# Kernel tuning notes

Measured on AMD Instinct MI355X. Metric: run time of the kernel, lower is better.

## Reference

```python
import jax, jax.numpy as jnp
import numpy as np

VOCAB = 50257
CH = 1024          # c_hidden_size = hidden_size(1020) + class_num(4)
LAT = 128
T = 1024
EOS = 1


def setup_inputs() -> dict:
    key = jax.random.key(0)
    ks = jax.random.split(key, 12)
    s = 0.02
    # tokens in [2, VOCAB) so EOS only appears at the final position
    toks = jax.random.randint(ks[0], (T,), 2, VOCAB, dtype=jnp.int32)
    input_tensor = toks.at[-1].set(EOS)
    inp = {
        "input_tensor": input_tensor,
        "h0": jnp.zeros((1, 1, CH), jnp.float32),
        "c0": jnp.zeros((1, 1, CH), jnp.float32),
        "eps": jax.random.normal(ks[1], (1, 1, LAT), jnp.float32),
        "emb": jax.random.normal(ks[2], (VOCAB, CH), jnp.float32) * s,
        "W_ih": jax.random.normal(ks[3], (4 * CH, CH), jnp.float32) * s,
        "W_hh": jax.random.normal(ks[4], (4 * CH, CH), jnp.float32) * s,
        "b_ih": jax.random.normal(ks[5], (4 * CH,), jnp.float32) * s,
        "b_hh": jax.random.normal(ks[6], (4 * CH,), jnp.float32) * s,
        "W_mean": jax.random.normal(ks[7], (LAT, 2 * CH), jnp.float32) * s,
        "b_mean": jnp.zeros((LAT,), jnp.float32),
        "W_logv": jax.random.normal(ks[8], (LAT, 2 * CH), jnp.float32) * s,
        "b_logv": jnp.zeros((LAT,), jnp.float32),
    }
    return inp


def reference(input_tensor, h0, c0, eps, emb, W_ih, W_hh, b_ih, b_hh,
              W_mean, b_mean, W_logv, b_logv):
    Tlen = input_tensor.shape[0]
    eos_idx = jnp.argmax(input_tensor == EOS)           # first EOS position
    active = jnp.arange(Tlen) < eos_idx                 # steps taken before break
    x_all = emb[input_tensor]                            # [T, CH]

    def step(carry, inp):
        h, c = carry
        x, a = inp
        gates = x @ W_ih.T + b_ih + h @ W_hh.T + b_hh    # [4*CH]
        i, f, g, o = jnp.split(gates, 4)                 # PyTorch LSTM gate order
        c_new = jax.nn.sigmoid(f) * c + jax.nn.sigmoid(i) * jnp.tanh(g)
        h_new = jax.nn.sigmoid(o) * jnp.tanh(c_new)
        h = jnp.where(a, h_new, h)
        c = jnp.where(a, c_new, c)
        return (h, c), None

    (h, c), _ = jax.lax.scan(step, (h0.reshape(-1), c0.reshape(-1)), (x_all, active))
    hc = jnp.concatenate([h, c])                         # cat((h, c), dim=2) flattened
    mean = hc @ W_mean.T + b_mean
    logv = hc @ W_logv.T + b_logv
    z = eps.reshape(-1) * jnp.exp(0.5 * logv) + mean     # reparameterize
    shp = (1, 1, LAT)
    return z.reshape(shp), mean.reshape(shp), logv.reshape(shp)
```

## Files before the change

### kernel.cpp

```cpp
#include <hip/hip_runtime.h>
#include <cstdint>
#include <cstddef>

#define T_LEN 1024
#define CH    1024
#define NGATE 4096
#define LAT   128
#define NBLK  128

#define WS_XG    0
#define WS_HBUF  (16777216)
#define WS_HFIN  (16777216 + 16384)
#define WS_CFIN  (16777216 + 24576)
#define WS_CTRL  (16777216 + 32768)

__device__ __forceinline__ float sigmf(float x) { return 1.0f / (1.0f + expf(-x)); }

__global__ __launch_bounds__(1024) void setup_k(const int* __restrict__ tok,
                                                int* __restrict__ ctrl) {
  __shared__ int red[1024];
  int tid = threadIdx.x;
  red[tid] = (tok[tid] == 1) ? tid : 0x7fffffff;
  __syncthreads();
  for (int s = 512; s > 0; s >>= 1) {
    if (tid < s) red[tid] = min(red[tid], red[tid + s]);
    __syncthreads();
  }
  if (tid == 0) {
    int e = red[0];
    ctrl[0] = (e == 0x7fffffff) ? 0 : e;
  }
}

__global__ __launch_bounds__(512) void xgemm_k(const int* __restrict__ tok,
                                               const float* __restrict__ emb,
                                               const float* __restrict__ Wih,
                                               const float* __restrict__ bih,
                                               const float* __restrict__ bhh,
                                               float* __restrict__ xg) {
  __shared__ float As[16 * 132];
  __shared__ float Bs[16 * 132];
  const int tid = threadIdx.x;
  const int r0 = blockIdx.x * 128;
  const int t0 = blockIdx.y * 128;
  const int tx = tid & 15, ty = tid >> 4;
  const int m0 = ty * 4, n0 = tx * 8;
  const int lrow = tid >> 2;
  const int kq   = (tid & 3) * 4;

  float acc[4][8];
#pragma unroll
  for (int i = 0; i < 4; i++)
#pragma unroll
    for (int j = 0; j < 8; j++) acc[i][j] = 0.0f;

  const int tokv = tok[t0 + lrow];
  const float* arow = emb + (size_t)tokv * CH;
  const float* brow = Wih + (size_t)(r0 + lrow) * CH;

  for (int k0 = 0; k0 < CH; k0 += 16) {
    float4 a4 = *(const float4*)(arow + k0 + kq);
    float4 b4 = *(const float4*)(brow + k0 + kq);
    __syncthreads();
    As[(kq + 0) * 132 + lrow] = a4.x;
    As[(kq + 1) * 132 + lrow] = a4.y;
    As[(kq + 2) * 132 + lrow] = a4.z;
    As[(kq + 3) * 132 + lrow] = a4.w;
    Bs[(kq + 0) * 132 + lrow] = b4.x;
    Bs[(kq + 1) * 132 + lrow] = b4.y;
    Bs[(kq + 2) * 132 + lrow] = b4.z;
    Bs[(kq + 3) * 132 + lrow] = b4.w;
    __syncthreads();
#pragma unroll
    for (int kk = 0; kk < 16; kk++) {
      float4 av = *(const float4*)&As[kk * 132 + m0];
      float4 b0 = *(const float4*)&Bs[kk * 132 + n0];
      float4 b1 = *(const float4*)&Bs[kk * 132 + n0 + 4];
      float aa[4] = {av.x, av.y, av.z, av.w};
      float bb[8] = {b0.x, b0.y, b0.z, b0.w, b1.x, b1.y, b1.z, b1.w};
#pragma unroll
      for (int i = 0; i < 4; i++)
#pragma unroll
        for (int j = 0; j < 8; j++) acc[i][j] += aa[i] * bb[j];
    }
  }

  float4 bi0 = *(const float4*)(bih + r0 + n0);
  float4 bi1 = *(const float4*)(bih + r0 + n0 + 4);
  float4 bh0 = *(const float4*)(bhh + r0 + n0);
  float4 bh1 = *(const float4*)(bhh + r0 + n0 + 4);
  float badd[8] = {bi0.x + bh0.x, bi0.y + bh0.y, bi0.z + bh0.z, bi0.w + bh0.w,
                   bi1.x + bh1.x, bi1.y + bh1.y, bi1.z + bh1.z, bi1.w + bh1.w};
#pragma unroll
  for (int i = 0; i < 4; i++) {
    float4 o0 = {acc[i][0] + badd[0], acc[i][1] + badd[1],
                 acc[i][2] + badd[2], acc[i][3] + badd[3]};
    float4 o1 = {acc[i][4] + badd[4], acc[i][5] + badd[5],
                 acc[i][6] + badd[6], acc[i][7] + badd[7]};
    float* dst = xg + (size_t)(t0 + m0 + i) * NGATE + r0 + n0;
    *(float4*)(dst) = o0;
    *(float4*)(dst + 4) = o1;
  }
}

__global__ __launch_bounds__(1024) void lstm_k(const float* __restrict__ h0,
                                               const float* __restrict__ c0,
                                               const float* __restrict__ eps,
                                               const float* __restrict__ Whh,
                                               const float* __restrict__ Wm,
                                               const float* __restrict__ bm,
                                               const float* __restrict__ Wl,
                                               const float* __restrict__ bl,
                                               const float* __restrict__ xg,
                                               unsigned long long* __restrict__ hbuf64,
                                               unsigned long long* __restrict__ hfin64,
                                               unsigned long long* __restrict__ cfin64,
                                               const int* __restrict__ ctrl,
                                               float* __restrict__ out) {
  __shared__ float hs[1024];
  __shared__ float hcs[2048];
  __shared__ float gv[32];
  __shared__ float rs[32];

  const int tid = threadIdx.x;
  const int b = blockIdx.x;
  const int g = tid >> 5, s = tid & 31;
  const int q = g >> 3, jj = g & 7;
  const int r = q * 1024 + b * 8 + jj;

  const float* wrow = Whh + (size_t)r * CH;
  float w[32];
#pragma unroll
  for (int i = 0; i < 32; i++) w[i] = wrow[s + 32 * i];

  const int eos = ctrl[0];

  float hreg = 0.0f, creg = 0.0f;
  if (tid < 8) { hreg = h0[b * 8 + tid]; creg = c0[b * 8 + tid]; }

  for (int t = 0; t < eos; t++) {
    float xv = 0.0f;
    if (s == 0) xv = xg[(size_t)t * NGATE + r];

    if (t == 0) {
      hs[tid] = h0[tid];
    } else {
      const unsigned want = (unsigned)t;
      const unsigned long long* src = hbuf64 + (size_t)(t & 1) * 1024 + tid;
      unsigned long long v;
      do {
        v = __hip_atomic_load(src, __ATOMIC_RELAXED, __HIP_MEMORY_SCOPE_AGENT);
      } while ((unsigned)(v >> 32) != want);
      hs[tid] = __uint_as_float((unsigned)(v & 0xffffffffu));
    }
    __syncthreads();

    float a0 = 0.0f, a1 = 0.0f;
#pragma unroll
    for (int i = 0; i < 32; i += 2) {
      a0 += w[i]     * hs[s + 32 * i];
      a1 += w[i + 1] * hs[s + 32 * (i + 1)];
    }
    float acc = a0 + a1;
    acc += __shfl_xor(acc, 16);
    acc += __shfl_xor(acc, 8);
    acc += __shfl_xor(acc, 4);
    acc += __shfl_xor(acc, 2);
    acc += __shfl_xor(acc, 1);
    if (s == 0) gv[g] = acc + xv;
    __syncthreads();

    if (tid < 8) {
      float iv = gv[tid], fv = gv[8 + tid], gg = gv[16 + tid], ov = gv[24 + tid];
      float cn = sigmf(fv) * creg + sigmf(iv) * tanhf(gg);
      float hn = sigmf(ov) * tanhf(cn);
      creg = cn; hreg = hn;
      unsigned long long pv = ((unsigned long long)(unsigned)(t + 1) << 32) |
                              (unsigned long long)__float_as_uint(hn);
      __hip_atomic_store(&hbuf64[(size_t)((t + 1) & 1) * 1024 + b * 8 + tid], pv,
                         __ATOMIC_RELAXED, __HIP_MEMORY_SCOPE_AGENT);
    }
  }

  if (tid < 8) {
    unsigned long long ph = (1ull << 32) | (unsigned long long)__float_as_uint(hreg);
    unsigned long long pc = (1ull << 32) | (unsigned long long)__float_as_uint(creg);
    __hip_atomic_store(&hfin64[b * 8 + tid], ph, __ATOMIC_RELAXED, __HIP_MEMORY_SCOPE_AGENT);
    __hip_atomic_store(&cfin64[b * 8 + tid], pc, __ATOMIC_RELAXED, __HIP_MEMORY_SCOPE_AGENT);
  }

  {
    unsigned long long vh, vc;
    do {
      vh = __hip_atomic_load(&hfin64[tid], __ATOMIC_RELAXED, __HIP_MEMORY_SCOPE_AGENT);
    } while ((unsigned)(vh >> 32) != 1u);
    do {
      vc = __hip_atomic_load(&cfin64[tid], __ATOMIC_RELAXED, __HIP_MEMORY_SCOPE_AGENT);
    } while ((unsigned)(vc >> 32) != 1u);
    hcs[tid] = __uint_as_float((unsigned)(vh & 0xffffffffu));
    hcs[1024 + tid] = __uint_as_float((unsigned)(vc & 0xffffffffu));
  }
  __syncthreads();

  float hc1 = hcs[tid];
  float hc2 = hcs[1024 + tid];
  float pm = Wm[(size_t)b * 2048 + tid] * hc1 + Wm[(size_t)b * 2048 + 1024 + tid] * hc2;
  float pl = Wl[(size_t)b * 2048 + tid] * hc1 + Wl[(size_t)b * 2048 + 1024 + tid] * hc2;
#pragma unroll
  for (int o = 32; o > 0; o >>= 1) {
    pm += __shfl_down(pm, o);
    pl += __shfl_down(pl, o);
  }
  const int wv = tid >> 6, ln = tid & 63;
  if (ln == 0) { rs[wv] = pm; rs[16 + wv] = pl; }
  __syncthreads();
  if (tid == 0) {
    float m = 0.0f, l = 0.0f;
    for (int i = 0; i < 16; i++) { m += rs[i]; l += rs[16 + i]; }
    m += bm[b];
    l += bl[b];
    float z = eps[b] * expf(0.5f * l) + m;
    out[b] = z;
    out[LAT + b] = m;
    out[2 * LAT + b] = l;
  }
}

extern "C" void kernel_launch(void* const* d_in, const int* in_sizes, int n_in,
                              void* d_out, int out_size, void* d_ws, size_t ws_size,
                              hipStream_t stream) {
  const int*   tok = (const int*)d_in[0];
  const float* h0  = (const float*)d_in[1];
  const float* c0  = (const float*)d_in[2];
  const float* eps = (const float*)d_in[3];
  const float* emb = (const float*)d_in[4];
  const float* Wih = (const float*)d_in[5];
  const float* Whh = (const float*)d_in[6];
  const float* bih = (const float*)d_in[7];
  const float* bhh = (const float*)d_in[8];
  const float* Wm  = (const float*)d_in[9];
  const float* bm  = (const float*)d_in[10];
  const float* Wl  = (const float*)d_in[11];
  const float* bl  = (const float*)d_in[12];
  float* out = (float*)d_out;

  char* ws = (char*)d_ws;
  float* xg = (float*)(ws + WS_XG);
  unsigned long long* hbuf64 = (unsigned long long*)(ws + WS_HBUF);
  unsigned long long* hfin64 = (unsigned long long*)(ws + WS_HFIN);
  unsigned long long* cfin64 = (unsigned long long*)(ws + WS_CFIN);
  int* ctrl = (int*)(ws + WS_CTRL);

  setup_k<<<1, 1024, 0, stream>>>(tok, ctrl);
  xgemm_k<<<dim3(NGATE / 128, T_LEN / 128), 512, 0, stream>>>(tok, emb, Wih, bih, bhh, xg);

  void* args[] = {(void*)&h0, (void*)&c0, (void*)&eps, (void*)&Whh,
                  (void*)&Wm, (void*)&bm, (void*)&Wl, (void*)&bl,
                  (void*)&xg, (void*)&hbuf64, (void*)&hfin64, (void*)&cfin64,
                  (void*)&ctrl, (void*)&out};
  hipLaunchCooperativeKernel((void*)lstm_k, dim3(NBLK), dim3(1024), args, 0, stream);
}
```

Before: 2.462 ms.

## Fuse input projection into persistent LSTM kernel with register-resident W_ih

Removes the separate input-projection GEMM and its 16MB xg buffer. W_ih rows are now held in registers next to W_hh inside the cooperative recurrent kernel. The x·W_ih dot for step t+1 is computed after the h exchange, and the embedding row for t+2 is prefetched. The recurrent kernel changes to 256 blocks of 256 threads, one gate column per wave with 16 lanes per gate, and each thread polls four h values at once. This trades a parallel GEMM for extra serial per-step work and high register pressure (128+64 floats per thread), which risks spills.

```diff
diff --git a/kernel.cpp b/kernel.cpp
--- a/kernel.cpp
+++ b/kernel.cpp
@@ -2,17 +2,14 @@
 #include <cstdint>
 #include <cstddef>
 
-#define T_LEN 1024
 #define CH    1024
-#define NGATE 4096
 #define LAT   128
-#define NBLK  128
-
-#define WS_XG    0
-#define WS_HBUF  (16777216)
-#define WS_HFIN  (16777216 + 16384)
-#define WS_CFIN  (16777216 + 24576)
-#define WS_CTRL  (16777216 + 32768)
+#define NBLK  256
+
+#define WS_HBUF  0
+#define WS_HFIN  16384
+#define WS_CFIN  (16384 + 8192)
+#define WS_CTRL  (16384 + 16384)
 
 __device__ __forceinline__ float sigmf(float x) { return 1.0f / (1.0f + expf(-x)); }
 
@@ -32,197 +29,210 @@
   }
 }
 
-__global__ __launch_bounds__(512) void xgemm_k(const int* __restrict__ tok,
-                                               const float* __restrict__ emb,
-                                               const float* __restrict__ Wih,
-                                               const float* __restrict__ bih,
-                                               const float* __restrict__ bhh,
-                                               float* __restrict__ xg) {
-  __shared__ float As[16 * 132];
-  __shared__ float Bs[16 * 132];
+__global__ __launch_bounds__(256, 1) void lstm_k(const int* __restrict__ tok,
+                                                 const float* __restrict__ h0,
+                                                 const float* __restrict__ c0,
+                                                 const float* __restrict__ eps,
+                                                 const float* __restrict__ emb,
+                                                 const float* __restrict__ Wih,
+                                                 const float* __restrict__ Whh,
+                                                 const float* __restrict__ bih,
+                                                 const float* __restrict__ bhh,
+                                                 const float* __restrict__ Wm,
+                                                 const float* __restrict__ bm,
+                                                 const float* __restrict__ Wl,
+                                                 const float* __restrict__ bl,
+                                                 unsigned long long* __restrict__ hbuf64,
+                                                 unsigned long long* __restrict__ hfin64,
+                                                 unsigned long long* __restrict__ cfin64,
+                                                 const int* __restrict__ ctrl,
+                                                 float* __restrict__ out) {
+  __shared__ float hs[2][1088];
+  __shared__ float hcs[2048];
+  __shared__ float rs[8];
+
   const int tid = threadIdx.x;
-  const int r0 = blockIdx.x * 128;
-  const int t0 = blockIdx.y * 128;
-  const int tx = tid & 15, ty = tid >> 4;
-  const int m0 = ty * 4, n0 = tx * 8;
-  const int lrow = tid >> 2;
-  const int kq   = (tid & 3) * 4;
-
-  float acc[4][8];
-#pragma unroll
-  for (int i = 0; i < 4; i++)
-#pragma unroll
-    for (int j = 0; j < 8; j++) acc[i][j] = 0.0f;
-
-  const int tokv = tok[t0 + lrow];
-  const float* arow = emb + (size_t)tokv * CH;
-  const float* brow = Wih + (size_t)(r0 + lrow) * CH;
-
-  for (int k0 = 0; k0 < CH; k0 += 16) {
-    float4 a4 = *(const float4*)(arow + k0 + kq);
-    float4 b4 = *(const float4*)(brow + k0 + kq);
-    __syncthreads();
-    As[(kq + 0) * 132 + lrow] = a4.x;
-    As[(kq + 1) * 132 + lrow] = a4.y;
-    As[(kq + 2) * 132 + lrow] = a4.z;
-    As[(kq + 3) * 132 + lrow] = a4.w;
-    Bs[(kq + 0) * 132 + lrow] = b4.x;
-    Bs[(kq + 1) * 132 + lrow] = b4.y;
-    Bs[(kq + 2) * 132 + lrow] = b4.z;
-    Bs[(kq + 3) * 132 + lrow] = b4.w;
-    __syncthreads();
-#pragma unroll
-    for (int kk = 0; kk < 16; kk++) {
-      float4 av = *(const float4*)&As[kk * 132 + m0];
-      float4 b0 = *(const float4*)&Bs[kk * 132 + n0];
-      float4 b1 = *(const float4*)&Bs[kk * 132 + n0 + 4];
-      float aa[4] = {av.x, av.y, av.z, av.w};
-      float bb[8] = {b0.x, b0.y, b0.z, b0.w, b1.x, b1.y, b1.z, b1.w};
-#pragma unroll
-      for (int i = 0; i < 4; i++)
-#pragma unroll
-        for (int j = 0; j < 8; j++) acc[i][j] += aa[i] * bb[j];
-    }
-  }
-
-  float4 bi0 = *(const float4*)(bih + r0 + n0);
-  float4 bi1 = *(const float4*)(bih + r0 + n0 + 4);
-  float4 bh0 = *(const float4*)(bhh + r0 + n0);
-  float4 bh1 = *(const float4*)(bhh + r0 + n0 + 4);
-  float badd[8] = {bi0.x + bh0.x, bi0.y + bh0.y, bi0.z + bh0.z, bi0.w + bh0.w,
-                   bi1.x + bh1.x, bi1.y + bh1.y, bi1.z + bh1.z, bi1.w + bh1.w};
-#pragma unroll
-  for (int i = 0; i < 4; i++) {
-    float4 o0 = {acc[i][0] + badd[0], acc[i][1] + badd[1],
-                 acc[i][2] + badd[2], acc[i][3] + badd[3]};
-    float4 o1 = {acc[i][4] + badd[4], acc[i][5] + badd[5],
-                 acc[i][6] + badd[6], acc[i][7] + badd[7]};
-    float* dst = xg + (size_t)(t0 + m0 + i) * NGATE + r0 + n0;
-    *(float4*)(dst) = o0;
-    *(float4*)(dst + 4) = o1;
-  }
-}
-
-__global__ __launch_bounds__(1024) void lstm_k(const float* __restrict__ h0,
-                                               const float* __restrict__ c0,
-                                               const float* __restrict__ eps,
-                                               const float* __restrict__ Whh,
-                                               const float* __restrict__ Wm,
-                                               const float* __restrict__ bm,
-                                               const float* __restrict__ Wl,
-                                               const float* __restrict__ bl,
-                                               const float* __restrict__ xg,
-                                               unsigned long long* __restrict__ hbuf64,
-                                               unsigned long long* __restrict__ hfin64,
-                                               unsigned long long* __restrict__ cfin64,
-                                               const int* __restrict__ ctrl,
-                                               float* __restrict__ out) {
-  __shared__ float hs[1024];
-  __shared__ float hcs[2048];
-  __shared__ float gv[32];
-  __shared__ float rs[32];
-
-  const int tid = threadIdx.x;
-  const int b = blockIdx.x;
-  const int g = tid >> 5, s = tid & 31;
-  const int q = g >> 3, jj = g & 7;
-  const int r = q * 1024 + b * 8 + jj;
-
-  const float* wrow = Whh + (size_t)r * CH;
-  float w[32];
-#pragma unroll
-  for (int i = 0; i < 32; i++) w[i] = wrow[s + 32 * i];
-
+  const int b   = blockIdx.x;
+  const int w   = tid >> 6;
+  const int l   = tid & 63;
+  const int q   = l >> 4;
+  const int m   = l & 15;
+  const int d   = b * 4 + w;
+  const int r   = q * 1024 + d;
+
+  float wh[64], wi[64];
+  {
+    const float* php = Whh + (size_t)r * CH + m * 64;
+    const float* pip = Wih + (size_t)r * CH + m * 64;
+#pragma unroll
+    for (int i = 0; i < 64; i += 4) {
+      float4 a = *(const float4*)(php + i);
+      wh[i] = a.x; wh[i + 1] = a.y; wh[i + 2] = a.z; wh[i + 3] = a.w;
+    }
+#pragma unroll
+    for (int i = 0; i < 64; i += 4) {
+      float4 a = *(const float4*)(pip + i);
+      wi[i] = a.x; wi[i + 1] = a.y; wi[i + 2] = a.z; wi[i + 3] = a.w;
+    }
+  }
+  const float binit = bih[r] + bhh[r];
   const int eos = ctrl[0];
 
-  float hreg = 0.0f, creg = 0.0f;
-  if (tid < 8) { hreg = h0[b * 8 + tid]; creg = c0[b * 8 + tid]; }
+  float creg = c0[d];
+  float hreg = h0[d];
+
+  float xreg[64];
+  float xacc = 0.0f;
+  {
+    const float* x0 = emb + (size_t)tok[0] * CH + m * 64;
+#pragma unroll
+    for (int i = 0; i < 64; i += 4) {
+      float4 a = *(const float4*)(x0 + i);
+      xacc += wi[i] * a.x + wi[i + 1] * a.y + wi[i + 2] * a.z + wi[i + 3] * a.w;
+    }
+    const float* x1 = emb + (size_t)tok[1] * CH + m * 64;
+#pragma unroll
+    for (int i = 0; i < 64; i += 4) {
+      float4 a = *(const float4*)(x1 + i);
+      xreg[i] = a.x; xreg[i + 1] = a.y; xreg[i + 2] = a.z; xreg[i + 3] = a.w;
+    }
+  }
 
   for (int t = 0; t < eos; t++) {
-    float xv = 0.0f;
-    if (s == 0) xv = xg[(size_t)t * NGATE + r];
-
+    float4 hv;
     if (t == 0) {
-      hs[tid] = h0[tid];
+      hv = *(const float4*)(h0 + tid * 4);
     } else {
       const unsigned want = (unsigned)t;
-      const unsigned long long* src = hbuf64 + (size_t)(t & 1) * 1024 + tid;
-      unsigned long long v;
+      const unsigned long long* src = hbuf64 + (size_t)(t & 1) * 1024 + tid * 4;
+      unsigned long long v0, v1, v2, v3;
+      bool ok;
       do {
-        v = __hip_atomic_load(src, __ATOMIC_RELAXED, __HIP_MEMORY_SCOPE_AGENT);
-      } while ((unsigned)(v >> 32) != want);
-      hs[tid] = __uint_as_float((unsigned)(v & 0xffffffffu));
-    }
+        v0 = __hip_atomic_load(src + 0, __ATOMIC_RELAXED, __HIP_MEMORY_SCOPE_AGENT);
+        v1 = __hip_atomic_load(src + 1, __ATOMIC_RELAXED, __HIP_MEMORY_SCOPE_AGENT);
+        v2 = __hip_atomic_load(src + 2, __ATOMIC_RELAXED, __HIP_MEMORY_SCOPE_AGENT);
+        v3 = __hip_atomic_load(src + 3, __ATOMIC_RELAXED, __HIP_MEMORY_SCOPE_AGENT);
+        ok = ((unsigned)(v0 >> 32) == want) & ((unsigned)(v1 >> 32) == want) &
+             ((unsigned)(v2 >> 32) == want) & ((unsigned)(v3 >> 32) == want);
+      } while (!ok);
+      hv.x = __uint_as_float((unsigned)v0);
+      hv.y = __uint_as_float((unsigned)v1);
+      hv.z = __uint_as_float((unsigned)v2);
+      hv.w = __uint_as_float((unsigned)v3);
+    }
+    *(float4*)&hs[t & 1][(tid >> 4) * 68 + (tid & 15) * 4] = hv;
     __syncthreads();
 
-    float a0 = 0.0f, a1 = 0.0f;
-#pragma unroll
-    for (int i = 0; i < 32; i += 2) {
-      a0 += w[i]     * hs[s + 32 * i];
-      a1 += w[i + 1] * hs[s + 32 * (i + 1)];
-    }
-    float acc = a0 + a1;
-    acc += __shfl_xor(acc, 16);
+    const float* hp = &hs[t & 1][m * 68];
+    float acc = xacc;
+#pragma unroll
+    for (int i = 0; i < 64; i += 4) {
+      float4 h4 = *(const float4*)(hp + i);
+      acc += wh[i] * h4.x + wh[i + 1] * h4.y + wh[i + 2] * h4.z + wh[i + 3] * h4.w;
+    }
+    acc += __shfl_xor(acc, 1);
+    acc += __shfl_xor(acc, 2);
+    acc += __shfl_xor(acc, 4);
     acc += __shfl_xor(acc, 8);
-    acc += __shfl_xor(acc, 4);
-    acc += __shfl_xor(acc, 2);
-    acc += __shfl_xor(acc, 1);
-    if (s == 0) gv[g] = acc + xv;
-    __syncthreads();
-
-    if (tid < 8) {
-      float iv = gv[tid], fv = gv[8 + tid], gg = gv[16 + tid], ov = gv[24 + tid];
-      float cn = sigmf(fv) * creg + sigmf(iv) * tanhf(gg);
-      float hn = sigmf(ov) * tanhf(cn);
-      creg = cn; hreg = hn;
+    float accb = acc + binit;
+    float iv = __shfl(accb, 0);
+    float fv = __shfl(accb, 16);
+    float gv = __shfl(accb, 32);
+    float ov = __shfl(accb, 48);
+    float cn = sigmf(fv) * creg + sigmf(iv) * tanhf(gv);
+    float hn = sigmf(ov) * tanhf(cn);
+    creg = cn;
+    hreg = hn;
+    if (l == 0) {
       unsigned long long pv = ((unsigned long long)(unsigned)(t + 1) << 32) |
                               (unsigned long long)__float_as_uint(hn);
-      __hip_atomic_store(&hbuf64[(size_t)((t + 1) & 1) * 1024 + b * 8 + tid], pv,
+      __hip_atomic_store(&hbuf64[(size_t)((t + 1) & 1) * 1024 + d], pv,
                          __ATOMIC_RELAXED, __HIP_MEMORY_SCOPE_AGENT);
     }
-  }
-
-  if (tid < 8) {
+
+    float xa = 0.0f;
+#pragma unroll
+    for (int i = 0; i < 64; i += 4)
+      xa += wi[i] * xreg[i] + wi[i + 1] * xreg[i + 1] +
+            wi[i + 2] * xreg[i + 2] + wi[i + 3] * xreg[i + 3];
+    xacc = xa;
+    const int tn = min(t + 2, 1023);
+    const float* xp = emb + (size_t)tok[tn] * CH + m * 64;
+#pragma unroll
+    for (int i = 0; i < 64; i += 4) {
+      float4 a = *(const float4*)(xp + i);
+      xreg[i] = a.x; xreg[i + 1] = a.y; xreg[i + 2] = a.z; xreg[i + 3] = a.w;
+    }
+  }
+
+  if (l == 0) {
     unsigned long long ph = (1ull << 32) | (unsigned long long)__float_as_uint(hreg);
     unsigned long long pc = (1ull << 32) | (unsigned long long)__float_as_uint(creg);
-    __hip_atomic_store(&hfin64[b * 8 + tid], ph, __ATOMIC_RELAXED, __HIP_MEMORY_SCOPE_AGENT);
-    __hip_atomic_store(&cfin64[b * 8 + tid], pc, __ATOMIC_RELAXED, __HIP_MEMORY_SCOPE_AGENT);
-  }
-
-  {
-    unsigned long long vh, vc;
+    __hip_atomic_store(&hfin64[d], ph, __ATOMIC_RELAXED, __HIP_MEMORY_SCOPE_AGENT);
+    __hip_atomic_store(&cfin64[d], pc, __ATOMIC_RELAXED, __HIP_MEMORY_SCOPE_AGENT);
+  }
+  if (b >= LAT) return;
+
+  {
+    const unsigned long long* hp = hfin64 + tid * 4;
+    const unsigned long long* cp = cfin64 + tid * 4;
+    unsigned long long v0, v1, v2, v3;
+    bool ok;
     do {
-      vh = __hip_atomic_load(&hfin64[tid], __ATOMIC_RELAXED, __HIP_MEMORY_SCOPE_AGENT);
-    } while ((unsigned)(vh >> 32) != 1u);
+      v0 = __hip_atomic_load(hp + 0, __ATOMIC_RELAXED, __HIP_MEMORY_SCOPE_AGENT);
+      v1 = __hip_atomic_load(hp + 1, __ATOMIC_RELAXED, __HIP_MEMORY_SCOPE_AGENT);
+      v2 = __hip_atomic_load(hp + 2, __ATOMIC_RELAXED, __HIP_MEMORY_SCOPE_AGENT);
+      v3 = __hip_atomic_load(hp + 3, __ATOMIC_RELAXED, __HIP_MEMORY_SCOPE_AGENT);
+      ok = ((unsigned)(v0 >> 32) == 1u) & ((unsigned)(v1 >> 32) == 1u) &
+           ((unsigned)(v2 >> 32) == 1u) & ((unsigned)(v3 >> 32) == 1u);
+    } while (!ok);
+    hcs[tid * 4 + 0] = __uint_as_float((unsigned)v0);
+    hcs[tid * 4 + 1] = __uint_as_float((unsigned)v1);
+    hcs[tid * 4 + 2] = __uint_as_float((unsigned)v2);
+    hcs[tid * 4 + 3] = __uint_as_float((unsigned)v3);
     do {
-      vc = __hip_atomic_load(&cfin64[tid], __ATOMIC_RELAXED, __HIP_MEMORY_SCOPE_AGENT);
-    } while ((unsigned)(vc >> 32) != 1u);
-    hcs[tid] = __uint_as_float((unsigned)(vh & 0xffffffffu));
-    hcs[1024 + tid] = __uint_as_float((unsigned)(vc & 0xffffffffu));
+      v0 = __hip_atomic_load(cp + 0, __ATOMIC_RELAXED, __HIP_MEMORY_SCOPE_AGENT);
+      v1 = __hip_atomic_load(cp + 1, __ATOMIC_RELAXED, __HIP_MEMORY_SCOPE_AGENT);
+      v2 = __hip_atomic_load(cp + 2, __ATOMIC_RELAXED, __HIP_MEMORY_SCOPE_AGENT);
+      v3 = __hip_atomic_load(cp + 3, __ATOMIC_RELAXED, __HIP_MEMORY_SCOPE_AGENT);
+      ok = ((unsigned)(v0 >> 32) == 1u) & ((unsigned)(v1 >> 32) == 1u) &
+           ((unsigned)(v2 >> 32) == 1u) & ((unsigned)(v3 >> 32) == 1u);
+    } while (!ok);
+    hcs[1024 + tid * 4 + 0] = __uint_as_float((unsigned)v0);
+    hcs[1024 + tid * 4 + 1] = __uint_as_float((unsigned)v1);
+    hcs[1024 + tid * 4 + 2] = __uint_as_float((unsigned)v2);
+    hcs[1024 + tid * 4 + 3] = __uint_as_float((unsigned)v3);
   }
   __syncthreads();
 
-  float hc1 = hcs[tid];
-  float hc2 = hcs[1024 + tid];
-  float pm = Wm[(size_t)b * 2048 + tid] * hc1 + Wm[(size_t)b * 2048 + 1024 + tid] * hc2;
-  float pl = Wl[(size_t)b * 2048 + tid] * hc1 + Wl[(size_t)b * 2048 + 1024 + tid] * hc2;
+  float pm = 0.0f, pl = 0.0f;
+  {
+    const float* wmp = Wm + (size_t)b * 2048 + tid * 8;
+    const float* wlp = Wl + (size_t)b * 2048 + tid * 8;
+    const float* hcp = &hcs[tid * 8];
+#pragma unroll
+    for (int j = 0; j < 8; j += 4) {
+      float4 wm4 = *(const float4*)(wmp + j);
+      float4 wl4 = *(const float4*)(wlp + j);
+      float4 hc4 = *(const float4*)(hcp + j);
+      pm += wm4.x * hc4.x + wm4.y * hc4.y + wm4.z * hc4.z + wm4.w * hc4.w;
+      pl += wl4.x * hc4.x + wl4.y * hc4.y + wl4.z * hc4.z + wl4.w * hc4.w;
+    }
+  }
 #pragma unroll
   for (int o = 32; o > 0; o >>= 1) {
     pm += __shfl_down(pm, o);
     pl += __shfl_down(pl, o);
   }
-  const int wv = tid >> 6, ln = tid & 63;
-  if (ln == 0) { rs[wv] = pm; rs[16 + wv] = pl; }
+  if (l == 0) { rs[w] = pm; rs[4 + w] = pl; }
   __syncthreads();
   if (tid == 0) {
-    float m = 0.0f, l = 0.0f;
-    for (int i = 0; i < 16; i++) { m += rs[i]; l += rs[16 + i]; }
-    m += bm[b];
-    l += bl[b];
-    float z = eps[b] * expf(0.5f * l) + m;
+    float mval = rs[0] + rs[1] + rs[2] + rs[3] + bm[b];
+    float lval = rs[4] + rs[5] + rs[6] + rs[7] + bl[b];
+    float z = eps[b] * expf(0.5f * lval) + mval;
     out[b] = z;
-    out[LAT + b] = m;
-    out[2 * LAT + b] = l;
+    out[LAT + b] = mval;
+    out[2 * LAT + b] = lval;
   }
 }
 
@@ -245,18 +255,17 @@
   float* out = (float*)d_out;
 
   char* ws = (char*)d_ws;
-  float* xg = (float*)(ws + WS_XG);
   unsigned long long* hbuf64 = (unsigned long long*)(ws + WS_HBUF);
   unsigned long long* hfin64 = (unsigned long long*)(ws + WS_HFIN);
   unsigned long long* cfin64 = (unsigned long long*)(ws + WS_CFIN);
   int* ctrl = (int*)(ws + WS_CTRL);
 
   setup_k<<<1, 1024, 0, stream>>>(tok, ctrl);
-  xgemm_k<<<dim3(NGATE / 128, T_LEN / 128), 512, 0, stream>>>(tok, emb, Wih, bih, bhh, xg);
-
-  void* args[] = {(void*)&h0, (void*)&c0, (void*)&eps, (void*)&Whh,
+
+  void* args[] = {(void*)&tok, (void*)&h0, (void*)&c0, (void*)&eps, (void*)&emb,
+                  (void*)&Wih, (void*)&Whh, (void*)&bih, (void*)&bhh,
                   (void*)&Wm, (void*)&bm, (void*)&Wl, (void*)&bl,
-                  (void*)&xg, (void*)&hbuf64, (void*)&hfin64, (void*)&cfin64,
+                  (void*)&hbuf64, (void*)&hfin64, (void*)&cfin64,
                   (void*)&ctrl, (void*)&out};
-  hipLaunchCooperativeKernel((void*)lstm_k, dim3(NBLK), dim3(1024), args, 0, stream);
+  hipLaunchCooperativeKernel((void*)lstm_k, dim3(NBLK), dim3(256), args, 0, stream);
 }
```

New measurement: 3.682 ms. +49.6%, slower.
